# Performance work log

Hardware: AMD Instinct MI355X
Metric: run time of the kernel (lower is better)

The kernel has to match this reference:

```python
import jax, jax.numpy as jnp
import numpy as np

NX, NY = 512, 512  # BEV grid size (init_kwargs nx, ny)


def setup_inputs() -> dict:
    key = jax.random.key(0)
    k_emb, k_coord, k_mask = jax.random.split(key, 3)
    B, P, C = 4, 12000, 64
    pillar_embeddings = jax.random.normal(k_emb, (B, P, C), dtype=jnp.float32)
    # unique grid cells per batch (real voxelization never maps two pillars to one cell)
    flat = jax.vmap(lambda k: jax.random.permutation(k, NX * NY)[:P])(
        jax.random.split(k_coord, B))
    pillar_coords = jnp.stack([flat % NX, flat // NX], axis=-1).astype(jnp.int32)  # (ix, iy)
    pillar_mask = jax.random.randint(k_mask, (B, P), 0, 2).astype(jnp.int32)
    return {"pillar_embeddings": pillar_embeddings,
            "pillar_coords": pillar_coords,
            "pillar_mask": pillar_mask}


def reference(pillar_embeddings, pillar_coords, pillar_mask):
    # pillar_embeddings: [B, P, C]; pillar_coords: [B, P, 2] (ix, iy); pillar_mask: [B, P]
    B, P, C = pillar_embeddings.shape
    flat = pillar_coords[..., 1] * NX + pillar_coords[..., 0]          # iy*nx + ix -> [B, P]
    # route invalid pillars to a dummy slot (index NX*NY) that is sliced off afterwards
    idx = jnp.where(pillar_mask > 0, flat, NX * NY)                    # [B, P]
    bev = jnp.zeros((B, NX * NY + 1, C), dtype=pillar_embeddings.dtype)
    bev = bev.at[jnp.arange(B)[:, None], idx].set(pillar_embeddings)   # vectorized scatter
    bev = bev[:, :NX * NY].reshape(B, NY, NX, C)
    return bev.transpose(0, 3, 1, 2)                                   # [B, C, NY, NX]
```

## Files before the change

### kernel.cpp

```cpp
#include <hip/hip_runtime.h>

#define NXc 512
#define NYc 512
#define Bc  4
#define Pc  12000
#define Cc  64

__global__ void bev_zero_kernel(float4* __restrict__ out, int n4) {
    int i = blockIdx.x * blockDim.x + threadIdx.x;
    int stride = gridDim.x * blockDim.x;
    const float4 z = make_float4(0.f, 0.f, 0.f, 0.f);
    for (; i < n4; i += stride) out[i] = z;
}

__global__ void bev_scatter_kernel(const float* __restrict__ emb,
                                   const int* __restrict__ coords,
                                   const int* __restrict__ mask,
                                   float* __restrict__ out) {
    const int wavesPerBlock = blockDim.x >> 6;
    const int pillar = blockIdx.x * wavesPerBlock + (threadIdx.x >> 6);
    const int lane = threadIdx.x & 63;
    if (pillar >= Bc * Pc) return;
    if (mask[pillar] <= 0) return;
    const int ix = coords[pillar * 2 + 0];
    const int iy = coords[pillar * 2 + 1];
    const int flat = iy * NXc + ix;
    const int b = pillar / Pc;
    const float v = emb[(size_t)pillar * Cc + lane];
    out[((size_t)b * Cc + lane) * (NYc * NXc) + flat] = v;
}

extern "C" void kernel_launch(void* const* d_in, const int* in_sizes, int n_in,
                              void* d_out, int out_size, void* d_ws, size_t ws_size,
                              hipStream_t stream) {
    const float* emb   = (const float*)d_in[0];
    const int* coords  = (const int*)d_in[1];
    const int* mask    = (const int*)d_in[2];
    float* out         = (float*)d_out;

    const int n4 = out_size >> 2;
    bev_zero_kernel<<<8192, 256, 0, stream>>>((float4*)out, n4);

    const int nPillars = Bc * Pc;
    const int pillarsPerBlock = 256 / 64;
    const int grid = (nPillars + pillarsPerBlock - 1) / pillarsPerBlock;
    bev_scatter_kernel<<<grid, 256, 0, stream>>>(emb, coords, mask, out);
}
```

Measured before the change: 330.6 us.

## Replace zero-fill plus scatter with index map and dense gather write

Instead of zero-filling the 256MB output and then scattering pillar channels with strided stores, builds a per-cell pillar index map in workspace (init to -1, scatter indices). A gather kernel then writes every output element exactly once with coalesced float4 nontemporal stores, reading embeddings for occupied cells and writing zeros otherwise. This removes the double write of touched lines and the uncoalesced scatter writes, at the cost of a 4MB map init/scatter pass and irregular embedding reads.

```diff
diff --git a/kernel.cpp b/kernel.cpp
--- a/kernel.cpp
+++ b/kernel.cpp
@@ -5,44 +5,69 @@
 #define Bc  4
 #define Pc  12000
 #define Cc  64
+#define CELLS (NXc * NYc)
+#define MAPN  (Bc * CELLS)
 
-__global__ void bev_zero_kernel(float4* __restrict__ out, int n4) {
-    int i = blockIdx.x * blockDim.x + threadIdx.x;
-    int stride = gridDim.x * blockDim.x;
-    const float4 z = make_float4(0.f, 0.f, 0.f, 0.f);
-    for (; i < n4; i += stride) out[i] = z;
+typedef float fv4 __attribute__((ext_vector_type(4)));
+typedef int   iv4 __attribute__((ext_vector_type(4)));
+
+__global__ void map_init_kernel(iv4* __restrict__ map4) {
+    const int i = blockIdx.x * blockDim.x + threadIdx.x;
+    iv4 m = {-1, -1, -1, -1};
+    map4[i] = m;
 }
 
-__global__ void bev_scatter_kernel(const float* __restrict__ emb,
-                                   const int* __restrict__ coords,
+__global__ void map_scatter_kernel(const int* __restrict__ coords,
                                    const int* __restrict__ mask,
-                                   float* __restrict__ out) {
-    const int wavesPerBlock = blockDim.x >> 6;
-    const int pillar = blockIdx.x * wavesPerBlock + (threadIdx.x >> 6);
-    const int lane = threadIdx.x & 63;
-    if (pillar >= Bc * Pc) return;
-    if (mask[pillar] <= 0) return;
-    const int ix = coords[pillar * 2 + 0];
-    const int iy = coords[pillar * 2 + 1];
-    const int flat = iy * NXc + ix;
-    const int b = pillar / Pc;
-    const float v = emb[(size_t)pillar * Cc + lane];
-    out[((size_t)b * Cc + lane) * (NYc * NXc) + flat] = v;
+                                   int* __restrict__ map) {
+    const int p = blockIdx.x * blockDim.x + threadIdx.x;
+    if (p >= Bc * Pc) return;
+    if (mask[p] <= 0) return;
+    const int ix = coords[2 * p];
+    const int iy = coords[2 * p + 1];
+    const int b = p / Pc;
+    map[b * CELLS + iy * NXc + ix] = p;
+}
+
+__global__ void __launch_bounds__(256)
+bev_gather_kernel(const float* __restrict__ emb,
+                  const iv4* __restrict__ map4,
+                  fv4* __restrict__ out4) {
+    const int t = blockIdx.x * blockDim.x + threadIdx.x;
+    const int x4 = t & (NXc / 4 - 1);
+    const int y  = (t >> 7) & (NYc - 1);
+    const int b  = t >> 16;
+    const iv4 m = map4[t];
+
+    const float* e0 = emb + (size_t)(m.x < 0 ? 0 : m.x) * Cc;
+    const float* e1 = emb + (size_t)(m.y < 0 ? 0 : m.y) * Cc;
+    const float* e2 = emb + (size_t)(m.z < 0 ? 0 : m.z) * Cc;
+    const float* e3 = emb + (size_t)(m.w < 0 ? 0 : m.w) * Cc;
+
+    fv4* op = out4 + (size_t)b * Cc * (CELLS / 4) + y * (NXc / 4) + x4;
+    #pragma unroll 8
+    for (int c = 0; c < Cc; ++c) {
+        fv4 v;
+        v.x = (m.x >= 0) ? e0[c] : 0.0f;
+        v.y = (m.y >= 0) ? e1[c] : 0.0f;
+        v.z = (m.z >= 0) ? e2[c] : 0.0f;
+        v.w = (m.w >= 0) ? e3[c] : 0.0f;
+        __builtin_nontemporal_store(v, op);
+        op += CELLS / 4;
+    }
 }
 
 extern "C" void kernel_launch(void* const* d_in, const int* in_sizes, int n_in,
                               void* d_out, int out_size, void* d_ws, size_t ws_size,
                               hipStream_t stream) {
-    const float* emb   = (const float*)d_in[0];
-    const int* coords  = (const int*)d_in[1];
-    const int* mask    = (const int*)d_in[2];
-    float* out         = (float*)d_out;
+    const float* emb  = (const float*)d_in[0];
+    const int* coords = (const int*)d_in[1];
+    const int* mask   = (const int*)d_in[2];
+    float* out        = (float*)d_out;
+    int* map          = (int*)d_ws;
 
-    const int n4 = out_size >> 2;
-    bev_zero_kernel<<<8192, 256, 0, stream>>>((float4*)out, n4);
-
-    const int nPillars = Bc * Pc;
-    const int pillarsPerBlock = 256 / 64;
-    const int grid = (nPillars + pillarsPerBlock - 1) / pillarsPerBlock;
-    bev_scatter_kernel<<<grid, 256, 0, stream>>>(emb, coords, mask, out);
+    map_init_kernel<<<MAPN / 4 / 256, 256, 0, stream>>>((iv4*)map);
+    map_scatter_kernel<<<(Bc * Pc + 255) / 256, 256, 0, stream>>>(coords, mask, map);
+    bev_gather_kernel<<<MAPN / 4 / 256, 256, 0, stream>>>(emb, (const iv4*)map,
+                                                          (fv4*)out);
 }
```

Result: faster. 284.4 us (-14.0%).
